# Performance work log

Measured on AMD Instinct MI355X. Metric: run time of the kernel, lower is better.

## Reference

```python
import jax, jax.numpy as jnp
import numpy as np

NUM_HEADS = 12
LN_EPS = 1e-5


def _layernorm(t, w, b):
    # LayerNorm over last dim (head_dim), biased variance as in torch
    mu = jnp.mean(t, axis=-1, keepdims=True)
    var = jnp.mean(jnp.square(t - mu), axis=-1, keepdims=True)
    return (t - mu) * jax.lax.rsqrt(var + LN_EPS) * w + b


def _apply_rope(t, cos, sin):
    # t: [B, H, S, D]; cos/sin: [S, D//2]; interleaved complex pairs (torch view_as_complex)
    tr = t[..., 0::2]
    ti = t[..., 1::2]
    c = cos[None, None, :, :]
    s = sin[None, None, :, :]
    out_r = tr * c - ti * s
    out_i = tr * s + ti * c
    return jnp.stack([out_r, out_i], axis=-1).reshape(t.shape)


def setup_inputs() -> dict:
    key = jax.random.key(0)
    ks = jax.random.split(key, 6)
    B, N, C = 16, 1024, 768
    H = NUM_HEADS
    D = C // H  # 64
    P, L = 1, 32
    rot_len = N - P - L  # 991
    x = jax.random.normal(ks[0], (B, N, C), dtype=jnp.float32)
    # rotary frequencies (llama-style)
    inv_freq = 1.0 / (10000.0 ** (np.arange(0, D, 2, dtype=np.float32) / D))
    angles = np.arange(rot_len, dtype=np.float32)[:, None] * inv_freq[None, :]
    cos = jnp.asarray(np.cos(angles))
    sin = jnp.asarray(np.sin(angles))
    # parameters (qkv_bias=False, qk_norm=True)
    w_qkv = jax.random.normal(ks[1], (C, 3 * C), dtype=jnp.float32) * (C ** -0.5)
    q_ln_w = jnp.ones((D,), jnp.float32)
    q_ln_b = jnp.zeros((D,), jnp.float32)
    k_ln_w = jnp.ones((D,), jnp.float32)
    k_ln_b = jnp.zeros((D,), jnp.float32)
    w_proj = jax.random.normal(ks[2], (C, C), dtype=jnp.float32) * (C ** -0.5)
    b_proj = jnp.zeros((C,), jnp.float32)
    return {
        "x": x, "cos": cos, "sin": sin,
        "w_qkv": w_qkv,
        "q_ln_w": q_ln_w, "q_ln_b": q_ln_b,
        "k_ln_w": k_ln_w, "k_ln_b": k_ln_b,
        "w_proj": w_proj, "b_proj": b_proj,
        "num_prefix_tokens": 1, "num_latent_tokens": 32,
    }


def reference(x, cos, sin, w_qkv, q_ln_w, q_ln_b, k_ln_w, k_ln_b, w_proj, b_proj,
              num_prefix_tokens, num_latent_tokens):
    B, N, C = x.shape
    H = NUM_HEADS
    D = C // H
    P, L = num_prefix_tokens, num_latent_tokens
    scale = D ** -0.5

    qkv = (x @ w_qkv).reshape(B, N, 3, H, D)
    qkv = jnp.transpose(qkv, (2, 0, 3, 1, 4))  # [3, B, H, N, D]
    q, k, v = qkv[0], qkv[1], qkv[2]

    q = _layernorm(q, q_ln_w, q_ln_b)
    k = _layernorm(k, k_ln_w, k_ln_b)

    # partial RoPE: only the middle [P : N-L] tokens are rotated
    q_rot = _apply_rope(q[:, :, P:N - L], cos, sin)
    k_rot = _apply_rope(k[:, :, P:N - L], cos, sin)
    q = jnp.concatenate([q[:, :, :P], q_rot, q[:, :, N - L:]], axis=2)
    k = jnp.concatenate([k[:, :, :P], k_rot, k[:, :, N - L:]], axis=2)

    attn = jnp.einsum("bhqd,bhkd->bhqk", q * scale, k)
    attn = jax.nn.softmax(attn, axis=-1)
    out = jnp.einsum("bhqk,bhkd->bhqd", attn, v)
    out = jnp.transpose(out, (0, 2, 1, 3)).reshape(B, N, C)
    return out @ w_proj + b_proj
```

## Files before the change

kernel.cpp:

```cpp
#include <hip/hip_runtime.h>
#include <hip/hip_bf16.h>

typedef __attribute__((ext_vector_type(8))) short v8s;
typedef __attribute__((ext_vector_type(4))) short v4s;
typedef __attribute__((ext_vector_type(4))) float f32x4;

__device__ __forceinline__ float bf2f(short s){
  unsigned u = ((unsigned)(unsigned short)s) << 16;
  float f; __builtin_memcpy(&f, &u, 4); return f;
}
__device__ __forceinline__ short f2bf(float f){
  unsigned u; __builtin_memcpy(&u, &f, 4);
  unsigned r = (u + 0x7FFFu + ((u >> 16) & 1u)) >> 16;
  return (short)r;
}
__device__ __forceinline__ unsigned cvtpk(float a, float b){
  unsigned r;
  asm("v_cvt_pk_bf16_f32 %0, %1, %2" : "=v"(r) : "v"(a), "v"(b));
  return r;
}

__device__ __forceinline__ void gload16(const void* g, void* l){
  __builtin_amdgcn_global_load_lds((const __attribute__((address_space(1))) void*)g,
                                   (__attribute__((address_space(3))) void*)l, 16, 0, 0);
}

__global__ __launch_bounds__(256) void k_cast8(const float* __restrict__ in,
                                               short* __restrict__ out, long n){
  long i = ((long)blockIdx.x * 256 + threadIdx.x) * 8;
  long stride = (long)gridDim.x * 256 * 8;
  for (; i < n; i += stride){
    float4 a = *(const float4*)(in + i);
    float4 b = *(const float4*)(in + i + 4);
    v8s v;
    v[0]=f2bf(a.x); v[1]=f2bf(a.y); v[2]=f2bf(a.z); v[3]=f2bf(a.w);
    v[4]=f2bf(b.x); v[5]=f2bf(b.y); v[6]=f2bf(b.z); v[7]=f2bf(b.w);
    *(v8s*)(out + i) = v;
  }
}

__global__ __launch_bounds__(256) void k_tcast(const float* __restrict__ in,
                                               short* __restrict__ out, int R, int Cc){
  __shared__ float T[32][33];
  int tx = threadIdx.x & 31, ty = threadIdx.x >> 5;
  int r0 = blockIdx.x * 32, c0 = blockIdx.y * 32;
  #pragma unroll
  for (int p = 0; p < 4; p++){
    int r = ty + p*8;
    T[r][tx] = in[(long)(r0 + r)*Cc + c0 + tx];
  }
  __syncthreads();
  #pragma unroll
  for (int p = 0; p < 4; p++){
    int r = ty + p*8;
    out[(long)(c0 + r)*R + r0 + tx] = f2bf(T[tx][r]);
  }
}

template<int OUT_MODE>
__global__ __launch_bounds__(256) void k_gemm(const short* __restrict__ A,
                                              const short* __restrict__ Bt,
                                              void* __restrict__ Cout,
                                              const float* __restrict__ bias,
                                              int M, int N, int K){
  __shared__ short As[128*64];
  __shared__ short Bs[128*64];
  int row0 = blockIdx.x * 128, col0 = blockIdx.y * 128;
  int t = threadIdx.x;
  int lane = t & 63, w = t >> 6;
  int g = lane >> 4, r16 = lane & 15;
  int wr = w >> 1, wc = w & 1;
  int rsw = (r16 & 7) << 3;
  int srow = t >> 3;
  int scol = ((t & 7) * 8) ^ ((srow & 7) << 3);
  f32x4 acc[4][4];
  #pragma unroll
  for (int mi = 0; mi < 4; mi++)
    #pragma unroll
    for (int ni = 0; ni < 4; ni++)
      acc[mi][ni] = (f32x4){0.f,0.f,0.f,0.f};

  for (int kt = 0; kt < K; kt += 64){
    #pragma unroll
    for (int p = 0; p < 4; p++){
      int rr = p*32 + srow;
      gload16(&A[(long)(row0 + rr)*K + kt + scol], &As[(p*256 + w*64)*8]);
    }
    #pragma unroll
    for (int p = 0; p < 4; p++){
      int rr = p*32 + srow;
      gload16(&Bt[(long)(col0 + rr)*K + kt + scol], &Bs[(p*256 + w*64)*8]);
    }
    __syncthreads();
    #pragma unroll
    for (int ks = 0; ks < 2; ks++){
      v8s af[4], bfr[4];
      #pragma unroll
      for (int mi = 0; mi < 4; mi++)
        af[mi] = *(const v8s*)&As[(wr*64 + mi*16 + r16)*64 + ((ks*32 + g*8) ^ rsw)];
      #pragma unroll
      for (int ni = 0; ni < 4; ni++)
        bfr[ni] = *(const v8s*)&Bs[(wc*64 + ni*16 + r16)*64 + ((ks*32 + g*8) ^ rsw)];
      __builtin_amdgcn_s_setprio(1);
      #pragma unroll
      for (int mi = 0; mi < 4; mi++)
        #pragma unroll
        for (int ni = 0; ni < 4; ni++)
          acc[mi][ni] = __builtin_amdgcn_mfma_f32_16x16x32_bf16(af[mi], bfr[ni], acc[mi][ni], 0, 0, 0);
      __builtin_amdgcn_s_setprio(0);
    }
    __syncthreads();
  }
  #pragma unroll
  for (int mi = 0; mi < 4; mi++)
    #pragma unroll
    for (int ni = 0; ni < 4; ni++){
      int rbase = row0 + wr*64 + mi*16 + g*4;
      int cc = col0 + wc*64 + ni*16 + r16;
      #pragma unroll
      for (int j = 0; j < 4; j++){
        float v = acc[mi][ni][j];
        if (OUT_MODE == 0)
          ((short*)Cout)[(long)(rbase + j)*N + cc] = f2bf(v);
        else
          ((float*)Cout)[(long)(rbase + j)*N + cc] = v + bias[cc];
      }
    }
}

__global__ __launch_bounds__(256) void k_lnrope(const short* __restrict__ QKV,
     const float* __restrict__ cosT, const float* __restrict__ sinT,
     const float* __restrict__ qw, const float* __restrict__ qb,
     const float* __restrict__ kw, const float* __restrict__ kb,
     short* __restrict__ Qb, short* __restrict__ Kb, short* __restrict__ Vt){
  __shared__ short Vs[64][72];
  int blk = blockIdx.x;
  int ntile = blk & 15, h = (blk >> 4) % 12, b = blk / 192;
  int t = threadIdx.x;
  int tl = t >> 2, ch = t & 3;
  int n = ntile*64 + tl;
  long row = (long)(b*1024 + n) * 2304;
  int d0 = ch * 16;
  long outrow = ((long)(b*12 + h)*1024 + n) * 64;

  #pragma unroll
  for (int sel = 0; sel < 2; sel++){
    const short* src = &QKV[row + sel*768 + h*64 + d0];
    float f[16];
    v8s a0 = *(const v8s*)src;
    v8s a1 = *(const v8s*)(src + 8);
    #pragma unroll
    for (int i = 0; i < 8; i++){ f[i] = bf2f(a0[i]); f[8+i] = bf2f(a1[i]); }
    float s1 = 0.f, s2 = 0.f;
    #pragma unroll
    for (int i = 0; i < 16; i++){ s1 += f[i]; s2 += f[i]*f[i]; }
    s1 += __shfl_xor(s1, 1); s2 += __shfl_xor(s2, 1);
    s1 += __shfl_xor(s1, 2); s2 += __shfl_xor(s2, 2);
    float mu = s1 * (1.0f/64.0f);
    float var = s2 * (1.0f/64.0f) - mu*mu;
    float rs = rsqrtf(var + 1e-5f);
    const float* wp = sel ? kw : qw;
    const float* bp = sel ? kb : qb;
    #pragma unroll
    for (int i = 0; i < 16; i++) f[i] = (f[i] - mu)*rs*wp[d0+i] + bp[d0+i];
    if (n >= 1 && n < 992){
      int pos = n - 1;
      const float* cp = &cosT[pos*32 + ch*8];
      const float* sp = &sinT[pos*32 + ch*8];
      #pragma unroll
      for (int i = 0; i < 8; i++){
        float c = cp[i], s = sp[i];
        float tr = f[2*i], ti = f[2*i+1];
        f[2*i]   = tr*c - ti*s;
        f[2*i+1] = tr*s + ti*c;
      }
    }
    if (sel == 0){
      #pragma unroll
      for (int i = 0; i < 16; i++) f[i] *= 0.18033688011112042f;
    }
    v8s o0, o1;
    #pragma unroll
    for (int i = 0; i < 8; i++){ o0[i] = f2bf(f[i]); o1[i] = f2bf(f[8+i]); }
    short* dst = sel ? &Kb[outrow + d0] : &Qb[outrow + d0];
    *(v8s*)dst = o0;
    *(v8s*)(dst + 8) = o1;
  }
  {
    const short* vsrc = &QKV[row + 1536 + h*64 + d0];
    *(v8s*)&Vs[tl][d0]     = *(const v8s*)vsrc;
    *(v8s*)&Vs[tl][d0 + 8] = *(const v8s*)(vsrc + 8);
  }
  __syncthreads();
  {
    int d = tl, nch = ch;
    v8s o0, o1;
    #pragma unroll
    for (int i = 0; i < 8; i++){ o0[i] = Vs[nch*16 + i][d]; o1[i] = Vs[nch*16 + 8 + i][d]; }
    long vbase = ((long)(b*12 + h)*64 + d)*1024 + ntile*64 + (nch>>1)*32 + (nch&1)*4;
    union { v8s s; v4s h2[2]; } u0, u1;
    u0.s = o0; u1.s = o1;
    *(v4s*)&Vt[vbase]      = u0.h2[0];
    *(v4s*)&Vt[vbase + 8]  = u0.h2[1];
    *(v4s*)&Vt[vbase + 16] = u1.h2[0];
    *(v4s*)&Vt[vbase + 24] = u1.h2[1];
  }
}

__global__ __launch_bounds__(512) void k_attn(const short* __restrict__ Qb,
                                              const short* __restrict__ Kb,
                                              const short* __restrict__ Vt,
                                              short* __restrict__ O){
  __shared__ short Ks[2][128*64];
  __shared__ short Vts[2][64*128];
  int blk = blockIdx.x;
  int qt = blk & 7, h = (blk >> 3) % 12, b = blk / 96;
  long bh = b*12 + h;
  int t = threadIdx.x, lane = t & 63, w = t >> 6;
  int g = lane >> 4, r16 = lane & 15;
  int rsw = (r16 & 7) << 3;
  int q0 = qt*128 + w*16;

  int srow = t >> 3;
  int scol = ((t & 7) * 8) ^ ((srow & 7) << 3);
  const short* KsrcB = &Kb[(bh*1024 + srow)*64 + scol];
  int sdv = t >> 4;
  int sslot = t & 15;
  int scolv = (sslot >> 3)*64 + (((sslot & 7)*8) ^ ((sdv & 7) << 3));
  const short* VsrcB = &Vt[(bh*64 + sdv)*1024 + scolv];
  int lbase = w*512;

  gload16(KsrcB,                 &Ks[0][lbase]);
  gload16(KsrcB + 4096,          &Ks[0][4096 + lbase]);
  gload16(VsrcB,                 &Vts[0][lbase]);
  gload16(VsrcB + 32768,         &Vts[0][4096 + lbase]);

  v8s bq[2];
  #pragma unroll
  for (int tt = 0; tt < 2; tt++)
    bq[tt] = *(const v8s*)&Qb[(bh*1024 + q0 + r16)*64 + tt*32 + g*8];

  f32x4 oacc[4];
  #pragma unroll
  for (int t2 = 0; t2 < 4; t2++) oacc[t2] = (f32x4){0.f,0.f,0.f,0.f};
  float m_run = -1e30f, l_part = 0.f;

  asm volatile("s_waitcnt vmcnt(0)" ::: "memory");
  __builtin_amdgcn_s_barrier();
  asm volatile("" ::: "memory");

  for (int it = 0; it < 8; ++it){
    int cur = it & 1;
    if (it < 7){
      int kt = (it + 1) * 128;
      gload16(KsrcB + (long)kt*64,          &Ks[cur^1][lbase]);
      gload16(KsrcB + (long)kt*64 + 4096,   &Ks[cur^1][4096 + lbase]);
      gload16(VsrcB + kt,                   &Vts[cur^1][lbase]);
      gload16(VsrcB + 32768 + kt,           &Vts[cur^1][4096 + lbase]);
    }
    const short* KsC  = &Ks[cur][0];
    const short* VtsC = &Vts[cur][0];

    #pragma unroll
    for (int sub = 0; sub < 2; sub++){
      int ksub = sub*4096;
      f32x4 sacc[4];
      #pragma unroll
      for (int f = 0; f < 4; f++) sacc[f] = (f32x4){0.f,0.f,0.f,0.f};
      #pragma unroll
      for (int tt = 0; tt < 2; tt++){
        v8s ak[4];
        #pragma unroll
        for (int f = 0; f < 4; f++)
          ak[f] = *(const v8s*)&KsC[ksub + (f*16 + r16)*64 + ((tt*32 + g*8) ^ rsw)];
        __builtin_amdgcn_s_setprio(1);
        #pragma unroll
        for (int f = 0; f < 4; f++)
          sacc[f] = __builtin_amdgcn_mfma_f32_16x16x32_bf16(ak[f], bq[tt], sacc[f], 0, 0, 0);
        __builtin_amdgcn_s_setprio(0);
      }
      float mf[4];
      #pragma unroll
      for (int f = 0; f < 4; f++)
        mf[f] = fmaxf(fmaxf(sacc[f][0], sacc[f][1]), fmaxf(sacc[f][2], sacc[f][3]));
      float mt_loc = fmaxf(fmaxf(mf[0], mf[1]), fmaxf(mf[2], mf[3]));
      if (!__all(mt_loc - m_run <= 8.0f)){
        float mt = fmaxf(mt_loc, __shfl_xor(mt_loc, 16));
        mt = fmaxf(mt, __shfl_xor(mt, 32));
        float m_new = fmaxf(m_run, mt);
        float alpha = exp2f(m_run - m_new);
        float aj4[4];
        #pragma unroll
        for (int j = 0; j < 4; j++) aj4[j] = __shfl(alpha, 4*g + j, 64);
        #pragma unroll
        for (int t2 = 0; t2 < 4; t2++)
          #pragma unroll
          for (int j = 0; j < 4; j++) oacc[t2][j] *= aj4[j];
        l_part *= alpha;
        m_run = m_new;
      }
      float p[4][4];
      float ls[4];
      #pragma unroll
      for (int f = 0; f < 4; f++){
        #pragma unroll
        for (int j = 0; j < 4; j++) p[f][j] = exp2f(sacc[f][j] - m_run);
        ls[f] = (p[f][0] + p[f][1]) + (p[f][2] + p[f][3]);
      }
      l_part += (ls[0] + ls[1]) + (ls[2] + ls[3]);

      unsigned d00 = cvtpk(p[0][0], p[0][1]), d01 = cvtpk(p[0][2], p[0][3]);
      unsigned d10 = cvtpk(p[1][0], p[1][1]), d11 = cvtpk(p[1][2], p[1][3]);
      unsigned d20 = cvtpk(p[2][0], p[2][1]), d21 = cvtpk(p[2][2], p[2][3]);
      unsigned d30 = cvtpk(p[3][0], p[3][1]), d31 = cvtpk(p[3][2], p[3][3]);
      union PU { v8s s; unsigned u[4]; };
      PU pa0, pa1;
      pa0.u[0]=d00; pa0.u[1]=d01; pa0.u[2]=d10; pa0.u[3]=d11;
      pa1.u[0]=d20; pa1.u[1]=d21; pa1.u[2]=d30; pa1.u[3]=d31;

      __builtin_amdgcn_s_setprio(1);
      #pragma unroll
      for (int t2 = 0; t2 < 4; t2++){
        int vrow = (t2*16 + r16)*128 + sub*64;
        #pragma unroll
        for (int kb = 0; kb < 2; kb++){
          v8s vbv = *(const v8s*)&VtsC[vrow + ((kb*32 + g*8) ^ rsw)];
          oacc[t2] = __builtin_amdgcn_mfma_f32_16x16x32_bf16(kb ? pa1.s : pa0.s, vbv, oacc[t2], 0, 0, 0);
        }
      }
      __builtin_amdgcn_s_setprio(0);
    }
    asm volatile("s_waitcnt vmcnt(0)" ::: "memory");
    __builtin_amdgcn_s_barrier();
    asm volatile("" ::: "memory");
  }
  float l_tot = l_part;
  l_tot += __shfl_xor(l_tot, 16);
  l_tot += __shfl_xor(l_tot, 32);
  float linv = 1.0f / l_tot;
  float lj[4];
  #pragma unroll
  for (int j = 0; j < 4; j++) lj[j] = __shfl(linv, 4*g + j, 64);
  #pragma unroll
  for (int t2 = 0; t2 < 4; t2++)
    #pragma unroll
    for (int j = 0; j < 4; j++){
      float v = oacc[t2][j] * lj[j];
      O[((long)b*1024 + q0 + 4*g + j)*768 + h*64 + t2*16 + r16] = f2bf(v);
    }
}

extern "C" void kernel_launch(void* const* d_in, const int* in_sizes, int n_in,
                              void* d_out, int out_size, void* d_ws, size_t ws_size,
                              hipStream_t stream) {
  const float* x      = (const float*)d_in[0];
  const float* cosT   = (const float*)d_in[1];
  const float* sinT   = (const float*)d_in[2];
  const float* w_qkv  = (const float*)d_in[3];
  const float* q_ln_w = (const float*)d_in[4];
  const float* q_ln_b = (const float*)d_in[5];
  const float* k_ln_w = (const float*)d_in[6];
  const float* k_ln_b = (const float*)d_in[7];
  const float* w_proj = (const float*)d_in[8];
  const float* b_proj = (const float*)d_in[9];

  char* ws = (char*)d_ws;
  short* Xb       = (short*)(ws);
  short* Wqkv_bt  = (short*)(ws + 25165824);
  short* Wproj_bt = (short*)(ws + 28704768);
  short* QKV      = (short*)(ws + 29884416);
  short* Qb       = (short*)(ws + 105381888);
  short* Kb       = (short*)(ws + 130547712);
  short* Vt       = (short*)(ws + 155713536);
  short* O        = (short*)(ws + 180879360);

  k_cast8<<<6144, 256, 0, stream>>>(x, Xb, 12582912L);
  k_tcast<<<dim3(24, 72), 256, 0, stream>>>(w_qkv, Wqkv_bt, 768, 2304);
  k_tcast<<<dim3(24, 24), 256, 0, stream>>>(w_proj, Wproj_bt, 768, 768);
  k_gemm<0><<<dim3(128, 18), 256, 0, stream>>>(Xb, Wqkv_bt, QKV, nullptr, 16384, 2304, 768);
  k_lnrope<<<3072, 256, 0, stream>>>(QKV, cosT, sinT, q_ln_w, q_ln_b, k_ln_w, k_ln_b, Qb, Kb, Vt);
  k_attn<<<1536, 512, 0, stream>>>(Qb, Kb, Vt, O);
  k_gemm<1><<<dim3(128, 6), 256, 0, stream>>>(O, Wproj_bt, d_out, b_proj, 16384, 768, 768);
}
```

Measured before the change: 354.8 us.

## Fuse QK LayerNorm and RoPE into the QKV GEMM epilogue

The QKV GEMM now applies per-head LayerNorm, RoPE and the Q scale in registers, reducing across lanes with shuffles, and writes Q and K directly in head-major bf16 layout. Only V is written to an intermediate buffer, which a slimmer kernel then transposes. This removes the round trip of Q and K through global memory and most of the separate LN/RoPE kernel. In exchange the epilogue gains shuffles and scattered 2-byte stores, plus cos/sin gathers per element.

Measured after the change: 365.2 us. 1.03x slower.

```diff
diff --git a/kernel.cpp b/kernel.cpp
--- a/kernel.cpp
+++ b/kernel.cpp
@@ -54,6 +54,128 @@
   for (int p = 0; p < 4; p++){
     int r = ty + p*8;
     out[(long)(c0 + r)*R + r0 + tx] = f2bf(T[tx][r]);
+  }
+}
+
+__global__ __launch_bounds__(256) void k_gemm_qkv(
+    const short* __restrict__ A, const short* __restrict__ Bt,
+    const float* __restrict__ cosT, const float* __restrict__ sinT,
+    const float* __restrict__ qw, const float* __restrict__ qb,
+    const float* __restrict__ kw, const float* __restrict__ kb,
+    short* __restrict__ Qb, short* __restrict__ Kb, short* __restrict__ Vraw){
+  __shared__ short As[128*64];
+  __shared__ short Bs[128*64];
+  const int K = 768;
+  int row0 = blockIdx.x * 128;
+  int by = blockIdx.y;
+  int col0 = by * 128;
+  int t = threadIdx.x;
+  int lane = t & 63, w = t >> 6;
+  int g = lane >> 4, r16 = lane & 15;
+  int wr = w >> 1, wc = w & 1;
+  int rsw = (r16 & 7) << 3;
+  int srow = t >> 3;
+  int scol = ((t & 7) * 8) ^ ((srow & 7) << 3);
+  f32x4 acc[4][4];
+  #pragma unroll
+  for (int mi = 0; mi < 4; mi++)
+    #pragma unroll
+    for (int ni = 0; ni < 4; ni++)
+      acc[mi][ni] = (f32x4){0.f,0.f,0.f,0.f};
+
+  for (int kt = 0; kt < K; kt += 64){
+    #pragma unroll
+    for (int p = 0; p < 4; p++){
+      int rr = p*32 + srow;
+      gload16(&A[(long)(row0 + rr)*K + kt + scol], &As[(p*256 + w*64)*8]);
+    }
+    #pragma unroll
+    for (int p = 0; p < 4; p++){
+      int rr = p*32 + srow;
+      gload16(&Bt[(long)(col0 + rr)*K + kt + scol], &Bs[(p*256 + w*64)*8]);
+    }
+    __syncthreads();
+    #pragma unroll
+    for (int ks = 0; ks < 2; ks++){
+      v8s af[4], bfr[4];
+      #pragma unroll
+      for (int mi = 0; mi < 4; mi++)
+        af[mi] = *(const v8s*)&As[(wr*64 + mi*16 + r16)*64 + ((ks*32 + g*8) ^ rsw)];
+      #pragma unroll
+      for (int ni = 0; ni < 4; ni++)
+        bfr[ni] = *(const v8s*)&Bs[(wc*64 + ni*16 + r16)*64 + ((ks*32 + g*8) ^ rsw)];
+      __builtin_amdgcn_s_setprio(1);
+      #pragma unroll
+      for (int mi = 0; mi < 4; mi++)
+        #pragma unroll
+        for (int ni = 0; ni < 4; ni++)
+          acc[mi][ni] = __builtin_amdgcn_mfma_f32_16x16x32_bf16(af[mi], bfr[ni], acc[mi][ni], 0, 0, 0);
+      __builtin_amdgcn_s_setprio(0);
+    }
+    __syncthreads();
+  }
+
+  bool isV = (by >= 12);
+  bool isQ = (by < 6);
+  int hh = (by % 6)*2 + wc;
+  if (isV){
+    #pragma unroll
+    for (int mi = 0; mi < 4; mi++)
+      #pragma unroll
+      for (int ni = 0; ni < 4; ni++){
+        int rbase = row0 + wr*64 + mi*16 + g*4;
+        int cc = (by - 12)*128 + wc*64 + ni*16 + r16;
+        #pragma unroll
+        for (int j = 0; j < 4; j++)
+          Vraw[(long)(rbase + j)*768 + cc] = f2bf(acc[mi][ni][j]);
+      }
+  } else {
+    const float* wp = isQ ? qw : kw;
+    const float* bp = isQ ? qb : kb;
+    short* outp = isQ ? Qb : Kb;
+    float wd[4], bd[4];
+    #pragma unroll
+    for (int ni = 0; ni < 4; ni++){ wd[ni] = wp[ni*16 + r16]; bd[ni] = bp[ni*16 + r16]; }
+    #pragma unroll
+    for (int mi = 0; mi < 4; mi++){
+      #pragma unroll
+      for (int j = 0; j < 4; j++){
+        float va[4] = {acc[mi][0][j], acc[mi][1][j], acc[mi][2][j], acc[mi][3][j]};
+        float s1 = (va[0] + va[1]) + (va[2] + va[3]);
+        float s2 = (va[0]*va[0] + va[1]*va[1]) + (va[2]*va[2] + va[3]*va[3]);
+        s1 += __shfl_xor(s1, 1); s2 += __shfl_xor(s2, 1);
+        s1 += __shfl_xor(s1, 2); s2 += __shfl_xor(s2, 2);
+        s1 += __shfl_xor(s1, 4); s2 += __shfl_xor(s2, 4);
+        s1 += __shfl_xor(s1, 8); s2 += __shfl_xor(s2, 8);
+        float mu = s1 * (1.0f/64.0f);
+        float var = s2 * (1.0f/64.0f) - mu*mu;
+        float rs = rsqrtf(var + 1e-5f);
+        int r = row0 + wr*64 + mi*16 + g*4 + j;
+        int b = r >> 10, n = r & 1023;
+        float vals[4];
+        #pragma unroll
+        for (int ni = 0; ni < 4; ni++) vals[ni] = (va[ni] - mu)*rs*wd[ni] + bd[ni];
+        bool rope = (n >= 1) && (n < 992);
+        int pos = rope ? (n - 1) : 0;
+        #pragma unroll
+        for (int ni = 0; ni < 4; ni++){
+          float pp = __shfl_xor(vals[ni], 1);
+          if (rope){
+            int i = (ni*16 + r16) >> 1;
+            float c = cosT[pos*32 + i], s = sinT[pos*32 + i];
+            vals[ni] = (r16 & 1) ? (pp*s + vals[ni]*c) : (vals[ni]*c - pp*s);
+          }
+        }
+        if (isQ){
+          #pragma unroll
+          for (int ni = 0; ni < 4; ni++) vals[ni] *= 0.18033688011112042f;
+        }
+        long obase = ((long)(b*12 + hh)*1024 + n)*64;
+        #pragma unroll
+        for (int ni = 0; ni < 4; ni++)
+          outp[obase + ni*16 + r16] = f2bf(vals[ni]);
+      }
+    }
   }
 }
 
@@ -120,91 +242,35 @@
       #pragma unroll
       for (int j = 0; j < 4; j++){
         float v = acc[mi][ni][j];
-        if (OUT_MODE == 0)
-          ((short*)Cout)[(long)(rbase + j)*N + cc] = f2bf(v);
-        else
-          ((float*)Cout)[(long)(rbase + j)*N + cc] = v + bias[cc];
-      }
-    }
-}
-
-__global__ __launch_bounds__(256) void k_lnrope(const short* __restrict__ QKV,
-     const float* __restrict__ cosT, const float* __restrict__ sinT,
-     const float* __restrict__ qw, const float* __restrict__ qb,
-     const float* __restrict__ kw, const float* __restrict__ kb,
-     short* __restrict__ Qb, short* __restrict__ Kb, short* __restrict__ Vt){
+        ((float*)Cout)[(long)(rbase + j)*N + cc] = v + bias[cc];
+      }
+    }
+}
+
+__global__ __launch_bounds__(256) void k_vtrans(const short* __restrict__ Vraw,
+                                                short* __restrict__ Vt){
   __shared__ short Vs[64][72];
   int blk = blockIdx.x;
   int ntile = blk & 15, h = (blk >> 4) % 12, b = blk / 192;
   int t = threadIdx.x;
   int tl = t >> 2, ch = t & 3;
   int n = ntile*64 + tl;
-  long row = (long)(b*1024 + n) * 2304;
   int d0 = ch * 16;
-  long outrow = ((long)(b*12 + h)*1024 + n) * 64;
-
-  #pragma unroll
-  for (int sel = 0; sel < 2; sel++){
-    const short* src = &QKV[row + sel*768 + h*64 + d0];
-    float f[16];
-    v8s a0 = *(const v8s*)src;
-    v8s a1 = *(const v8s*)(src + 8);
-    #pragma unroll
-    for (int i = 0; i < 8; i++){ f[i] = bf2f(a0[i]); f[8+i] = bf2f(a1[i]); }
-    float s1 = 0.f, s2 = 0.f;
-    #pragma unroll
-    for (int i = 0; i < 16; i++){ s1 += f[i]; s2 += f[i]*f[i]; }
-    s1 += __shfl_xor(s1, 1); s2 += __shfl_xor(s2, 1);
-    s1 += __shfl_xor(s1, 2); s2 += __shfl_xor(s2, 2);
-    float mu = s1 * (1.0f/64.0f);
-    float var = s2 * (1.0f/64.0f) - mu*mu;
-    float rs = rsqrtf(var + 1e-5f);
-    const float* wp = sel ? kw : qw;
-    const float* bp = sel ? kb : qb;
-    #pragma unroll
-    for (int i = 0; i < 16; i++) f[i] = (f[i] - mu)*rs*wp[d0+i] + bp[d0+i];
-    if (n >= 1 && n < 992){
-      int pos = n - 1;
-      const float* cp = &cosT[pos*32 + ch*8];
-      const float* sp = &sinT[pos*32 + ch*8];
-      #pragma unroll
-      for (int i = 0; i < 8; i++){
-        float c = cp[i], s = sp[i];
-        float tr = f[2*i], ti = f[2*i+1];
-        f[2*i]   = tr*c - ti*s;
-        f[2*i+1] = tr*s + ti*c;
-      }
-    }
-    if (sel == 0){
-      #pragma unroll
-      for (int i = 0; i < 16; i++) f[i] *= 0.18033688011112042f;
-    }
-    v8s o0, o1;
-    #pragma unroll
-    for (int i = 0; i < 8; i++){ o0[i] = f2bf(f[i]); o1[i] = f2bf(f[8+i]); }
-    short* dst = sel ? &Kb[outrow + d0] : &Qb[outrow + d0];
-    *(v8s*)dst = o0;
-    *(v8s*)(dst + 8) = o1;
-  }
-  {
-    const short* vsrc = &QKV[row + 1536 + h*64 + d0];
-    *(v8s*)&Vs[tl][d0]     = *(const v8s*)vsrc;
-    *(v8s*)&Vs[tl][d0 + 8] = *(const v8s*)(vsrc + 8);
-  }
+  const short* vsrc = &Vraw[(long)(b*1024 + n)*768 + h*64 + d0];
+  *(v8s*)&Vs[tl][d0]     = *(const v8s*)vsrc;
+  *(v8s*)&Vs[tl][d0 + 8] = *(const v8s*)(vsrc + 8);
   __syncthreads();
-  {
-    int d = tl, nch = ch;
-    v8s o0, o1;
-    #pragma unroll
-    for (int i = 0; i < 8; i++){ o0[i] = Vs[nch*16 + i][d]; o1[i] = Vs[nch*16 + 8 + i][d]; }
-    long vbase = ((long)(b*12 + h)*64 + d)*1024 + ntile*64 + (nch>>1)*32 + (nch&1)*4;
-    union { v8s s; v4s h2[2]; } u0, u1;
-    u0.s = o0; u1.s = o1;
-    *(v4s*)&Vt[vbase]      = u0.h2[0];
-    *(v4s*)&Vt[vbase + 8]  = u0.h2[1];
-    *(v4s*)&Vt[vbase + 16] = u1.h2[0];
-    *(v4s*)&Vt[vbase + 24] = u1.h2[1];
-  }
+  int d = tl, nch = ch;
+  v8s o0, o1;
+  #pragma unroll
+  for (int i = 0; i < 8; i++){ o0[i] = Vs[nch*16 + i][d]; o1[i] = Vs[nch*16 + 8 + i][d]; }
+  long vbase = ((long)(b*12 + h)*64 + d)*1024 + ntile*64 + (nch>>1)*32 + (nch&1)*4;
+  union { v8s s; v4s h2[2]; } u0, u1;
+  u0.s = o0; u1.s = o1;
+  *(v4s*)&Vt[vbase]      = u0.h2[0];
+  *(v4s*)&Vt[vbase + 8]  = u0.h2[1];
+  *(v4s*)&Vt[vbase + 16] = u1.h2[0];
+  *(v4s*)&Vt[vbase + 24] = u1.h2[1];
 }
 
 __global__ __launch_bounds__(512) void k_attn(const short* __restrict__ Qb,
@@ -368,7 +434,7 @@
   short* Xb       = (short*)(ws);
   short* Wqkv_bt  = (short*)(ws + 25165824);
   short* Wproj_bt = (short*)(ws + 28704768);
-  short* QKV      = (short*)(ws + 29884416);
+  short* Vraw     = (short*)(ws + 29884416);
   short* Qb       = (short*)(ws + 105381888);
   short* Kb       = (short*)(ws + 130547712);
   short* Vt       = (short*)(ws + 155713536);
@@ -377,8 +443,10 @@
   k_cast8<<<6144, 256, 0, stream>>>(x, Xb, 12582912L);
   k_tcast<<<dim3(24, 72), 256, 0, stream>>>(w_qkv, Wqkv_bt, 768, 2304);
   k_tcast<<<dim3(24, 24), 256, 0, stream>>>(w_proj, Wproj_bt, 768, 768);
-  k_gemm<0><<<dim3(128, 18), 256, 0, stream>>>(Xb, Wqkv_bt, QKV, nullptr, 16384, 2304, 768);
-  k_lnrope<<<3072, 256, 0, stream>>>(QKV, cosT, sinT, q_ln_w, q_ln_b, k_ln_w, k_ln_b, Qb, Kb, Vt);
+  k_gemm_qkv<<<dim3(128, 18), 256, 0, stream>>>(Xb, Wqkv_bt, cosT, sinT,
+                                                q_ln_w, q_ln_b, k_ln_w, k_ln_b,
+                                                Qb, Kb, Vraw);
+  k_vtrans<<<3072, 256, 0, stream>>>(Vraw, Vt);
   k_attn<<<1536, 512, 0, stream>>>(Qb, Kb, Vt, O);
   k_gemm<1><<<dim3(128, 6), 256, 0, stream>>>(O, Wproj_bt, d_out, b_proj, 16384, 768, 768);
 }
```
